# Performance work log

Measured on AMD Instinct MI355X. Metric: run time of the kernel, lower is better.

## Reference

```python
import jax, jax.numpy as jnp
import numpy as np

DT = 1.0 / 120.0
B, T = 2048, 2048


def setup_inputs() -> dict:
    key = jax.random.key(0)
    k1, k2 = jax.random.split(key)
    # friction, damping, restitution (restitution only affects the collision
    # branch, which is not exercised by the non-colliding reference dynamics)
    params = jax.random.uniform(k1, (3,), jnp.float32, 0.05, 0.9)
    # smooth synthetic trajectories: cumulative small steps of [x, y, theta]
    meas = jnp.cumsum(jax.random.normal(k2, (B, T, 3), jnp.float32) * 0.01, axis=1)
    return {"params": params, "measurements": meas}


def _ekf_loss(params, measurements):
    friction, damping = params[0], params[1]
    dt = jnp.asarray(DT, measurements.dtype)
    dtype = measurements.dtype

    R = jnp.diag(jnp.array([2.5e-7, 2.5e-7, 9.1e-3], dtype=dtype))
    Q = jnp.diag(jnp.array([2e-10, 2e-10, 3e-7, 3e-7, 1e-2, 1e-1], dtype=dtype))
    H = jnp.zeros((3, 6), dtype=dtype).at[0, 0].set(1.0).at[1, 1].set(1.0).at[2, 4].set(1.0)
    I6 = jnp.eye(6, dtype=dtype)

    # linearized transition Jacobian (constant-velocity with table damping)
    F = I6
    F = F.at[0, 2].set(dt).at[1, 3].set(dt).at[4, 5].set(dt)
    F = F.at[2, 2].set(1.0 - dt * damping).at[3, 3].set(1.0 - dt * damping)

    def predict_state(s):
        x, y, dx, dy, th, dth = s
        dx2 = dx - dt * (damping * dx + friction * jnp.sign(dx))
        dy2 = dy - dt * (damping * dy + friction * jnp.sign(dy))
        return jnp.stack([x + dx * dt, y + dy * dt, dx2, dy2, th + dth * dt, dth])

    def step(carry, z):
        s, P, acc = carry
        s_pred = predict_state(s)                     # (6,)
        P_pred = F @ P @ F.T + Q                      # (6,6)
        yv = z - H @ s_pred                           # (3,) innovation
        S = H @ P_pred @ H.T + R                      # (3,3)
        Sinv_y = jnp.linalg.solve(S, yv)
        K = jnp.linalg.solve(S.T, (P_pred @ H.T).T).T  # P_pred H^T S^{-1}
        s_new = s_pred + K @ yv
        P_new = (I6 - K @ H) @ P_pred
        # evaluation term: sign*exp(logdet(S)) + y^T S^{-1} y == det(S) + y^T S^{-1} y
        acc = acc + jnp.linalg.det(S) + yv @ Sinv_y
        return (s_new, P_new, acc), None

    def run_one(zs):
        # initial state from finite-difference velocities (as in the source)
        v0 = (zs[1] - zs[0]) / dt
        s0 = jnp.stack([zs[0, 0], zs[0, 1], v0[0], v0[1], zs[0, 2], v0[2]])
        P0 = I6 * 0.01
        (_, _, acc), _ = jax.lax.scan(step, (s0, P0, jnp.zeros((), dtype)), zs[1:])
        return acc / (zs.shape[0] - 1)

    return jnp.mean(jax.vmap(run_one)(measurements))


def reference(params, measurements):
    return _ekf_loss(params, measurements)
```

## Files before the change

kernel.cpp:

```cpp
#include <hip/hip_runtime.h>

#define DTF (1.0f/120.0f)

constexpr int Bn = 2048, Tn = 2048, NS = Tn - 1, ZF = Tn * 3;
constexpr int NCH = 16, LCH = 128;
constexpr int SPAN = 208;
constexpr int BT = 64;
constexpr int GX = Bn / BT;
constexpr int NBLK = GX * NCH;
constexpr int RING = 6;
constexpr int FR_F = 24;
constexpr int SLOT_F = BT * FR_F;

__global__ __launch_bounds__(BT, 2) void ekf_main(const float* __restrict__ params,
                                                  const float* __restrict__ meas,
                                                  double* __restrict__ part)
{
    __shared__ __align__(16) float lds[RING * SLOT_F];
    const int tid = threadIdx.x;
    const int B = blockIdx.x;
    const int m = (B & 7) * 64 + (B >> 3);
    const int g = m >> 4, c = m & 15;

    const float dt = DTF;
    const float fric = params[0];
    const float damping = params[1];
    const float a = 1.f - dt * damping;
    const float dfr = dt * fric;
    const float dt2 = dt * dt, a2 = a * a;
    const float qp = 2e-10f, qv = 3e-7f, qth = 1e-2f, qdth = 1e-1f;
    const float Rp = 2.5e-7f, Rt = 9.1e-3f;
    const char* __restrict__ ztb = (const char*)(meas + (size_t)(g * BT) * ZF);

    const int j0 = c * LCH;
    const int jend = min(j0 + LCH, NS);
    int jw = jend - SPAN;
    jw = (jw < 3) ? 0 : (jw - ((jw - 3) & 3));
    const int A0f = (3 * jw) & ~3;
    const int d = 3 * jw + 3 - A0f;
    const int r0 = j0 - jw, r1 = jend - jw;
    const bool head = (jw == 0);

    int Gbase[6], u16[6];
    #pragma unroll
    for (int i = 0; i < 6; ++i) {
        int U = i * 64 + tid;
        int rowL = U / 6, u = U - rowL * 6;
        int G = (rowL & 15) * 4 + (rowL >> 4);
        Gbase[i] = G * (ZF * 4);
        u16[i] = u * 16;
    }
    const int rbase = ((tid & 3) * 16 + (tid >> 2)) * FR_F;

#define ISSUE(F) do { \
    int As4_ = (A0f + 24 * (F)) * 4; \
    float* dst_ = &lds[((F) % RING) * SLOT_F]; \
    _Pragma("unroll") \
    for (int i_ = 0; i_ < 6; ++i_) { \
        int inrow_ = min(As4_ + u16[i_], (ZF - 4) * 4); \
        __builtin_amdgcn_global_load_lds((const void*)(ztb + Gbase[i_] + inrow_), \
                                         (void*)(dst_ + i_ * 256), 16, 0, 0); \
    } } while (0)

    ISSUE(0); ISSUE(1); ISSUE(2); ISSUE(3); ISSUE(4);

    float ckx0, ckx1, ckt0, ckt1, cisx, cist, cdet;
    {
        float x00=0.01f, x01=0.f, x11=0.01f, t00=0.01f, t01=0.f, t11=0.01f;
        for (int t = 0; t < 48; ++t) {
            float Pp00 = fmaf(dt2, x11, fmaf(2.f*dt, x01, x00)) + qp;
            float Pp01 = a * fmaf(dt, x11, x01);
            float Pp11 = fmaf(a2, x11, qv);
            float Sx = Pp00 + Rp, isx = __builtin_amdgcn_rcpf(Sx);
            float kx0 = Pp00*isx, kx1 = Pp01*isx;
            x00 = Pp00-kx0*Pp00; x01 = Pp01-kx0*Pp01; x11 = Pp11-kx1*Pp01;
            float Tp00 = fmaf(dt2, t11, fmaf(2.f*dt, t01, t00)) + qth;
            float Tp01 = fmaf(dt, t11, t01);
            float Tp11 = t11 + qdth;
            float St = Tp00 + Rt, ist = __builtin_amdgcn_rcpf(St);
            float kt0 = Tp00*ist, kt1 = Tp01*ist;
            t00 = Tp00-kt0*Tp00; t01 = Tp01-kt0*Tp01; t11 = Tp11-kt1*Tp01;
            ckx0=kx0; ckx1=kx1; ckt0=kt0; ckt1=kt1; cisx=isx; cist=ist; cdet=Sx*Sx*St;
        }
    }

    asm volatile("s_waitcnt vmcnt(24)" ::: "memory");
    __builtin_amdgcn_sched_barrier(0);

    const int ib = d - 3;
    float b0 = lds[rbase+ib], b1 = lds[rbase+ib+1], b2 = lds[rbase+ib+2];
    float b3 = lds[rbase+ib+3], b4 = lds[rbase+ib+4], b5 = lds[rbase+ib+5];
    float s0 = b0, s1 = b1, s4 = b2;
    float s2 = (b3-b0)/dt, s3 = (b4-b1)/dt, s5 = (b5-b2)/dt;

    float facc = 0.f, accP = 0.f, accT = 0.f;
    int nown = 0;
    float hx00=0.01f, hx01=0.f, hx11=0.01f, ht00=0.01f, ht01=0.f, ht11=0.01f;

    for (int s = 0;; ++s) {
        ISSUE(s + 5);
        asm volatile("s_waitcnt vmcnt(24)" ::: "memory");
        __builtin_amdgcn_sched_barrier(0);
        const float* sA = &lds[(s % RING) * SLOT_F + rbase];
        const float* sB = &lds[((s + 1) % RING) * SLOT_F + rbase];
        float zv[24];
        if (!head) {
            float4 v0 = *(const float4*)(sA + 4);
            float4 v1 = *(const float4*)(sA + 8);
            float4 v2 = *(const float4*)(sA + 12);
            float4 v3 = *(const float4*)(sA + 16);
            float4 v4 = *(const float4*)(sA + 20);
            float4 v5 = *(const float4*)(sB);
            zv[0]=v0.x; zv[1]=v0.y; zv[2]=v0.z; zv[3]=v0.w;
            zv[4]=v1.x; zv[5]=v1.y; zv[6]=v1.z; zv[7]=v1.w;
            zv[8]=v2.x; zv[9]=v2.y; zv[10]=v2.z; zv[11]=v2.w;
            zv[12]=v3.x; zv[13]=v3.y; zv[14]=v3.z; zv[15]=v3.w;
            zv[16]=v4.x; zv[17]=v4.y; zv[18]=v4.z; zv[19]=v4.w;
            zv[20]=v5.x; zv[21]=v5.y; zv[22]=v5.z; zv[23]=v5.w;
            #pragma unroll
            for (int ss = 0; ss < 8; ++ss) {
                float p0 = fmaf(dt, s2, s0), p1 = fmaf(dt, s3, s1), p4 = fmaf(dt, s5, s4);
                float p2 = fmaf(a, s2, -copysignf(dfr, s2));
                float p3 = fmaf(a, s3, -copysignf(dfr, s3));
                float y0 = zv[3*ss]-p0, y1 = zv[3*ss+1]-p1, y2 = zv[3*ss+2]-p4;
                s0 = fmaf(ckx0, y0, p0); s1 = fmaf(ckx0, y1, p1);
                s2 = fmaf(ckx1, y0, p2); s3 = fmaf(ckx1, y1, p3);
                s4 = fmaf(ckt0, y2, p4); s5 = fmaf(ckt1, y2, s5);
                int r = 8*s + ss;
                if (r >= r0 && r < r1) {
                    accP = fmaf(y0, y0, fmaf(y1, y1, accP));
                    accT = fmaf(y2, y2, accT);
                    ++nown;
                }
            }
        } else {
            #pragma unroll
            for (int k = 0; k < 21; ++k) zv[k] = sA[3 + k];
            zv[21] = sB[0]; zv[22] = sB[1]; zv[23] = sB[2];
            #pragma unroll
            for (int ss = 0; ss < 8; ++ss) {
                float Pp00 = fmaf(dt2, hx11, fmaf(2.f*dt, hx01, hx00)) + qp;
                float Pp01 = a * fmaf(dt, hx11, hx01);
                float Pp11 = fmaf(a2, hx11, qv);
                float Sx = Pp00 + Rp, isx = __builtin_amdgcn_rcpf(Sx);
                float kx0 = Pp00*isx, kx1 = Pp01*isx;
                hx00 = Pp00-kx0*Pp00; hx01 = Pp01-kx0*Pp01; hx11 = Pp11-kx1*Pp01;
                float Tp00 = fmaf(dt2, ht11, fmaf(2.f*dt, ht01, ht00)) + qth;
                float Tp01 = fmaf(dt, ht11, ht01);
                float Tp11 = ht11 + qdth;
                float St = Tp00 + Rt, ist = __builtin_amdgcn_rcpf(St);
                float kt0 = Tp00*ist, kt1 = Tp01*ist;
                ht00 = Tp00-kt0*Tp00; ht01 = Tp01-kt0*Tp01; ht11 = Tp11-kt1*Tp01;
                float p0 = fmaf(dt, s2, s0), p1 = fmaf(dt, s3, s1), p4 = fmaf(dt, s5, s4);
                float p2 = fmaf(a, s2, -copysignf(dfr, s2));
                float p3 = fmaf(a, s3, -copysignf(dfr, s3));
                float y0 = zv[3*ss]-p0, y1 = zv[3*ss+1]-p1, y2 = zv[3*ss+2]-p4;
                s0 = fmaf(kx0, y0, p0); s1 = fmaf(kx0, y1, p1);
                s2 = fmaf(kx1, y0, p2); s3 = fmaf(kx1, y1, p3);
                s4 = fmaf(kt0, y2, p4); s5 = fmaf(kt1, y2, s5);
                int r = 8*s + ss;
                if (r >= r0 && r < r1)
                    facc += Sx*Sx*St + isx*fmaf(y0, y0, y1*y1) + ist*y2*y2;
            }
        }
        if (8 * (s + 1) >= r1) break;
    }
    asm volatile("s_waitcnt vmcnt(0)" ::: "memory");
#undef ISSUE

    if (!head) facc = (float)nown * cdet + cisx * accP + cist * accT;

    double acc = (double)facc;
    for (int off = 32; off; off >>= 1) acc += __shfl_down(acc, off);
    if (tid == 0) part[m] = acc;
}

__global__ void finalize_kernel(const double* __restrict__ part, float* __restrict__ out)
{
    const int tid = threadIdx.x;
    double v = part[tid];
    for (int off = 32; off; off >>= 1) v += __shfl_down(v, off);
    __shared__ double wp[8];
    if ((tid & 63) == 0) wp[tid >> 6] = v;
    __syncthreads();
    if (tid == 0) {
        double t = 0.0;
        #pragma unroll
        for (int i = 0; i < 8; ++i) t += wp[i];
        out[0] = (float)(t / ((double)Bn * (double)NS));
    }
}

extern "C" void kernel_launch(void* const* d_in, const int* in_sizes, int n_in,
                              void* d_out, int out_size, void* d_ws, size_t ws_size,
                              hipStream_t stream)
{
    const float* params = (const float*)d_in[0];
    const float* meas = (const float*)d_in[1];
    double* part = (double*)d_ws;
    float* out = (float*)d_out;

    hipLaunchKernelGGL(ekf_main, dim3(NBLK), dim3(BT), 0, stream, params, meas, part);
    hipLaunchKernelGGL(finalize_kernel, dim3(1), dim3(512), 0, stream, part, out);
}
```

Before: 37.31 us.

## Share one staged measurement window between two waves per block with swizzled LDS

Blocks now have two wavefronts, and both consume the same 64-trajectory measurement window staged in LDS through a three-slot ring of 96-float frames. Each wave handles an overlapping 64-step sub-chunk with its own warm-up start, which shrinks the redundant warm-up span compared with the old 208-step window per 128-step chunk. The LDS layout uses an XOR swizzle so per-lane float4 reads avoid bank conflicts. The cost is block-level barriers around each frame, a cross-wave reduction, and uneven work between the exact head wave and the steady-state waves.

```diff
diff --git a/kernel.cpp b/kernel.cpp
--- a/kernel.cpp
+++ b/kernel.cpp
@@ -3,66 +3,56 @@
 #define DTF (1.0f/120.0f)
 
 constexpr int Bn = 2048, Tn = 2048, NS = Tn - 1, ZF = Tn * 3;
-constexpr int NCH = 16, LCH = 128;
-constexpr int SPAN = 208;
-constexpr int BT = 64;
-constexpr int GX = Bn / BT;
-constexpr int NBLK = GX * NCH;
-constexpr int RING = 6;
-constexpr int FR_F = 24;
-constexpr int SLOT_F = BT * FR_F;
+constexpr int NSUP = 16;
+constexpr int BT = 128;
+constexpr int NG = Bn / 64;
+constexpr int NBLK = NG * NSUP;
+constexpr int SLOT_F = 64 * 96;
 
 __global__ __launch_bounds__(BT, 2) void ekf_main(const float* __restrict__ params,
                                                   const float* __restrict__ meas,
                                                   double* __restrict__ part)
 {
-    __shared__ __align__(16) float lds[RING * SLOT_F];
-    const int tid = threadIdx.x;
+    __shared__ __align__(16) float lds[3 * SLOT_F];
+    __shared__ double wsum[2];
+
+    const int tid = threadIdx.x, wid = tid >> 6, lane = tid & 63;
     const int B = blockIdx.x;
-    const int m = (B & 7) * 64 + (B >> 3);
-    const int g = m >> 4, c = m & 15;
-
-    const float dt = DTF;
-    const float fric = params[0];
-    const float damping = params[1];
-    const float a = 1.f - dt * damping;
-    const float dfr = dt * fric;
+    const int g = (B & 7) + 8 * ((B >> 3) >> 4);
+    const int S = (B >> 3) & 15;
+    const int jz = 128 * S;
+    const int T_S = (S == 15) ? 4 : 6;
+
+    const float dt = DTF, fric = params[0], damping = params[1];
+    const float a = 1.f - dt * damping, dfr = dt * fric;
     const float dt2 = dt * dt, a2 = a * a;
     const float qp = 2e-10f, qv = 3e-7f, qth = 1e-2f, qdth = 1e-1f;
     const float Rp = 2.5e-7f, Rt = 9.1e-3f;
-    const char* __restrict__ ztb = (const char*)(meas + (size_t)(g * BT) * ZF);
-
-    const int j0 = c * LCH;
-    const int jend = min(j0 + LCH, NS);
-    int jw = jend - SPAN;
-    jw = (jw < 3) ? 0 : (jw - ((jw - 3) & 3));
-    const int A0f = (3 * jw) & ~3;
-    const int d = 3 * jw + 3 - A0f;
-    const int r0 = j0 - jw, r1 = jend - jw;
-    const bool head = (jw == 0);
-
-    int Gbase[6], u16[6];
+    const char* __restrict__ zb = (const char*)(meas + (size_t)g * 64 * ZF);
+
+    const bool exact = (S == 0 && wid == 0);
+    const int mst   = (S == 0 && wid == 1) ? 33 : (1 + 64 * wid);
+    const int mown0 = (S == 0) ? (wid ? 96 : 1) : (64 * (wid + 1));
+    const int mown1 = min((S == 0) ? (wid ? 192 : 96) : (64 * (wid + 2)), 2048 - jz);
+
+    int rbyte[12];
     #pragma unroll
-    for (int i = 0; i < 6; ++i) {
-        int U = i * 64 + tid;
-        int rowL = U / 6, u = U - rowL * 6;
-        int G = (rowL & 15) * 4 + (rowL >> 4);
-        Gbase[i] = G * (ZF * 4);
-        u16[i] = u * 16;
-    }
-    const int rbase = ((tid & 3) * 16 + (tid >> 2)) * FR_F;
+    for (int i = 0; i < 12; ++i) {
+        int ig = 12 * wid + i, C = 64 * ig + lane;
+        int r = C / 24, c = C - 24 * r;
+        rbyte[i] = r * (ZF * 4) + ((c ^ (r & 7)) * 16);
+    }
 
 #define ISSUE(F) do { \
-    int As4_ = (A0f + 24 * (F)) * 4; \
-    float* dst_ = &lds[((F) % RING) * SLOT_F]; \
+    int foff_ = (3 * jz + 96 * (F)) * 4; \
+    float* db_ = &lds[((F) % 3) * SLOT_F + wid * 12 * 256]; \
     _Pragma("unroll") \
-    for (int i_ = 0; i_ < 6; ++i_) { \
-        int inrow_ = min(As4_ + u16[i_], (ZF - 4) * 4); \
-        __builtin_amdgcn_global_load_lds((const void*)(ztb + Gbase[i_] + inrow_), \
-                                         (void*)(dst_ + i_ * 256), 16, 0, 0); \
-    } } while (0)
-
-    ISSUE(0); ISSUE(1); ISSUE(2); ISSUE(3); ISSUE(4);
+    for (int i_ = 0; i_ < 12; ++i_) \
+        __builtin_amdgcn_global_load_lds((const void*)(zb + rbyte[i_] + foff_), \
+                                         (void*)(db_ + i_ * 256), 16, 0, 0); \
+} while (0)
+
+    ISSUE(0); ISSUE(1); ISSUE(2);
 
     float ckx0, ckx1, ckt0, ckt1, cisx, cist, cdet;
     {
@@ -84,95 +74,100 @@
         }
     }
 
-    asm volatile("s_waitcnt vmcnt(24)" ::: "memory");
-    __builtin_amdgcn_sched_barrier(0);
-
-    const int ib = d - 3;
-    float b0 = lds[rbase+ib], b1 = lds[rbase+ib+1], b2 = lds[rbase+ib+2];
-    float b3 = lds[rbase+ib+3], b4 = lds[rbase+ib+4], b5 = lds[rbase+ib+5];
-    float s0 = b0, s1 = b1, s4 = b2;
-    float s2 = (b3-b0)/dt, s3 = (b4-b1)/dt, s5 = (b5-b2)/dt;
-
-    float facc = 0.f, accP = 0.f, accT = 0.f;
+    float s0=0.f,s1=0.f,s2=0.f,s3=0.f,s4=0.f,s5=0.f;
+    float hx00=0.01f,hx01=0.f,hx11=0.01f,ht00=0.01f,ht01=0.f,ht11=0.01f;
+    float facc=0.f, accP=0.f, accT=0.f;
     int nown = 0;
-    float hx00=0.01f, hx01=0.f, hx11=0.01f, ht00=0.01f, ht01=0.f, ht11=0.01f;
-
-    for (int s = 0;; ++s) {
-        ISSUE(s + 5);
-        asm volatile("s_waitcnt vmcnt(24)" ::: "memory");
-        __builtin_amdgcn_sched_barrier(0);
-        const float* sA = &lds[(s % RING) * SLOT_F + rbase];
-        const float* sB = &lds[((s + 1) % RING) * SLOT_F + rbase];
-        float zv[24];
-        if (!head) {
-            float4 v0 = *(const float4*)(sA + 4);
-            float4 v1 = *(const float4*)(sA + 8);
-            float4 v2 = *(const float4*)(sA + 12);
-            float4 v3 = *(const float4*)(sA + 16);
-            float4 v4 = *(const float4*)(sA + 20);
-            float4 v5 = *(const float4*)(sB);
-            zv[0]=v0.x; zv[1]=v0.y; zv[2]=v0.z; zv[3]=v0.w;
-            zv[4]=v1.x; zv[5]=v1.y; zv[6]=v1.z; zv[7]=v1.w;
-            zv[8]=v2.x; zv[9]=v2.y; zv[10]=v2.z; zv[11]=v2.w;
-            zv[12]=v3.x; zv[13]=v3.y; zv[14]=v3.z; zv[15]=v3.w;
-            zv[16]=v4.x; zv[17]=v4.y; zv[18]=v4.z; zv[19]=v4.w;
-            zv[20]=v5.x; zv[21]=v5.y; zv[22]=v5.z; zv[23]=v5.w;
-            #pragma unroll
-            for (int ss = 0; ss < 8; ++ss) {
-                float p0 = fmaf(dt, s2, s0), p1 = fmaf(dt, s3, s1), p4 = fmaf(dt, s5, s4);
-                float p2 = fmaf(a, s2, -copysignf(dfr, s2));
-                float p3 = fmaf(a, s3, -copysignf(dfr, s3));
-                float y0 = zv[3*ss]-p0, y1 = zv[3*ss+1]-p1, y2 = zv[3*ss+2]-p4;
-                s0 = fmaf(ckx0, y0, p0); s1 = fmaf(ckx0, y1, p1);
-                s2 = fmaf(ckx1, y0, p2); s3 = fmaf(ckx1, y1, p3);
-                s4 = fmaf(ckt0, y2, p4); s5 = fmaf(ckt1, y2, s5);
-                int r = 8*s + ss;
-                if (r >= r0 && r < r1) {
-                    accP = fmaf(y0, y0, fmaf(y1, y1, accP));
-                    accT = fmaf(y2, y2, accT);
-                    ++nown;
-                }
+    bool inited = false;
+    const int rx = lane & 7;
+
+#define PRED_UPD(KX0,KX1,KT0,KT1,Z0,Z1,Z2) \
+    float p0=fmaf(dt,s2,s0), p1=fmaf(dt,s3,s1), p4=fmaf(dt,s5,s4); \
+    float p2=fmaf(a,s2,-copysignf(dfr,s2)), p3=fmaf(a,s3,-copysignf(dfr,s3)); \
+    float y0=(Z0)-p0, y1=(Z1)-p1, y2=(Z2)-p4; \
+    s0=fmaf(KX0,y0,p0); s1=fmaf(KX0,y1,p1); s2=fmaf(KX1,y0,p2); s3=fmaf(KX1,y1,p3); \
+    s4=fmaf(KT0,y2,p4); s5=fmaf(KT1,y2,s5);
+
+#define TSTEP(K,Z0,Z1,Z2) { int m=m0+(K); if (m>=mst && m<mown1) { \
+    PRED_UPD(ckx0,ckx1,ckt0,ckt1,Z0,Z1,Z2) \
+    if (m>=mown0) { accP=fmaf(y0,y0,fmaf(y1,y1,accP)); accT=fmaf(y2,y2,accT); ++nown; } } }
+
+#define XSTEP(K,Z0,Z1,Z2) { int m=m0+(K); if (m>=mst && m<mown1) { \
+    float Pp00=fmaf(dt2,hx11,fmaf(2.f*dt,hx01,hx00))+qp; \
+    float Pp01=a*fmaf(dt,hx11,hx01); \
+    float Pp11=fmaf(a2,hx11,qv); \
+    float Sx=Pp00+Rp, isx=__builtin_amdgcn_rcpf(Sx); \
+    float kx0=Pp00*isx, kx1=Pp01*isx; \
+    hx00=Pp00-kx0*Pp00; hx01=Pp01-kx0*Pp01; hx11=Pp11-kx1*Pp01; \
+    float Tp00=fmaf(dt2,ht11,fmaf(2.f*dt,ht01,ht00))+qth; \
+    float Tp01=fmaf(dt,ht11,ht01); \
+    float Tp11=ht11+qdth; \
+    float St=Tp00+Rt, ist=__builtin_amdgcn_rcpf(St); \
+    float kt0=Tp00*ist, kt1=Tp01*ist; \
+    ht00=Tp00-kt0*Tp00; ht01=Tp01-kt0*Tp01; ht11=Tp11-kt1*Tp01; \
+    PRED_UPD(kx0,kx1,kt0,kt1,Z0,Z1,Z2) \
+    facc += Sx*Sx*St + isx*fmaf(y0,y0,y1*y1) + ist*y2*y2; } }
+
+#define READ6() \
+    float4 v0=*(const float4*)&fb[4*((cb+0)^rx)]; \
+    float4 v1=*(const float4*)&fb[4*((cb+1)^rx)]; \
+    float4 v2=*(const float4*)&fb[4*((cb+2)^rx)]; \
+    float4 v3=*(const float4*)&fb[4*((cb+3)^rx)]; \
+    float4 v4=*(const float4*)&fb[4*((cb+4)^rx)]; \
+    float4 v5=*(const float4*)&fb[4*((cb+5)^rx)]; \
+    if (!inited && m0 == mst-1) { \
+        s0=v0.x; s1=v0.y; s4=v0.z; \
+        s2=(v0.w-v0.x)/dt; s3=(v1.x-v0.y)/dt; s5=(v1.y-v0.z)/dt; inited=true; }
+
+    for (int f = 0; f < T_S; ++f) {
+        if (f <= T_S-3)      asm volatile("s_waitcnt vmcnt(24)" ::: "memory");
+        else if (f == T_S-2) asm volatile("s_waitcnt vmcnt(12)" ::: "memory");
+        else                 asm volatile("s_waitcnt vmcnt(0)"  ::: "memory");
+        __builtin_amdgcn_sched_barrier(0);
+        __builtin_amdgcn_s_barrier();
+        __builtin_amdgcn_sched_barrier(0);
+
+        const float* fb = &lds[(f % 3) * SLOT_F + lane * 96];
+        if (exact) {
+            for (int u = 0; u < 4; ++u) {
+                int m0 = 32*f + 8*u, cb = 6*u;
+                if (m0 + 8 <= mst-1 || m0 >= mown1) continue;
+                READ6()
+                XSTEP(0, v0.x,v0.y,v0.z)  XSTEP(1, v0.w,v1.x,v1.y)
+                XSTEP(2, v1.z,v1.w,v2.x)  XSTEP(3, v2.y,v2.z,v2.w)
+                XSTEP(4, v3.x,v3.y,v3.z)  XSTEP(5, v3.w,v4.x,v4.y)
+                XSTEP(6, v4.z,v4.w,v5.x)  XSTEP(7, v5.y,v5.z,v5.w)
             }
         } else {
-            #pragma unroll
-            for (int k = 0; k < 21; ++k) zv[k] = sA[3 + k];
-            zv[21] = sB[0]; zv[22] = sB[1]; zv[23] = sB[2];
-            #pragma unroll
-            for (int ss = 0; ss < 8; ++ss) {
-                float Pp00 = fmaf(dt2, hx11, fmaf(2.f*dt, hx01, hx00)) + qp;
-                float Pp01 = a * fmaf(dt, hx11, hx01);
-                float Pp11 = fmaf(a2, hx11, qv);
-                float Sx = Pp00 + Rp, isx = __builtin_amdgcn_rcpf(Sx);
-                float kx0 = Pp00*isx, kx1 = Pp01*isx;
-                hx00 = Pp00-kx0*Pp00; hx01 = Pp01-kx0*Pp01; hx11 = Pp11-kx1*Pp01;
-                float Tp00 = fmaf(dt2, ht11, fmaf(2.f*dt, ht01, ht00)) + qth;
-                float Tp01 = fmaf(dt, ht11, ht01);
-                float Tp11 = ht11 + qdth;
-                float St = Tp00 + Rt, ist = __builtin_amdgcn_rcpf(St);
-                float kt0 = Tp00*ist, kt1 = Tp01*ist;
-                ht00 = Tp00-kt0*Tp00; ht01 = Tp01-kt0*Tp01; ht11 = Tp11-kt1*Tp01;
-                float p0 = fmaf(dt, s2, s0), p1 = fmaf(dt, s3, s1), p4 = fmaf(dt, s5, s4);
-                float p2 = fmaf(a, s2, -copysignf(dfr, s2));
-                float p3 = fmaf(a, s3, -copysignf(dfr, s3));
-                float y0 = zv[3*ss]-p0, y1 = zv[3*ss+1]-p1, y2 = zv[3*ss+2]-p4;
-                s0 = fmaf(kx0, y0, p0); s1 = fmaf(kx0, y1, p1);
-                s2 = fmaf(kx1, y0, p2); s3 = fmaf(kx1, y1, p3);
-                s4 = fmaf(kt0, y2, p4); s5 = fmaf(kt1, y2, s5);
-                int r = 8*s + ss;
-                if (r >= r0 && r < r1)
-                    facc += Sx*Sx*St + isx*fmaf(y0, y0, y1*y1) + ist*y2*y2;
+            for (int u = 0; u < 4; ++u) {
+                int m0 = 32*f + 8*u, cb = 6*u;
+                if (m0 + 8 <= mst-1 || m0 >= mown1) continue;
+                READ6()
+                TSTEP(0, v0.x,v0.y,v0.z)  TSTEP(1, v0.w,v1.x,v1.y)
+                TSTEP(2, v1.z,v1.w,v2.x)  TSTEP(3, v2.y,v2.z,v2.w)
+                TSTEP(4, v3.x,v3.y,v3.z)  TSTEP(5, v3.w,v4.x,v4.y)
+                TSTEP(6, v4.z,v4.w,v5.x)  TSTEP(7, v5.y,v5.z,v5.w)
             }
         }
-        if (8 * (s + 1) >= r1) break;
+        __builtin_amdgcn_sched_barrier(0);
+        __builtin_amdgcn_s_barrier();
+        __builtin_amdgcn_sched_barrier(0);
+        if (f + 3 < T_S) ISSUE(f + 3);
     }
     asm volatile("s_waitcnt vmcnt(0)" ::: "memory");
+
+#undef READ6
+#undef XSTEP
+#undef TSTEP
+#undef PRED_UPD
 #undef ISSUE
 
-    if (!head) facc = (float)nown * cdet + cisx * accP + cist * accT;
-
-    double acc = (double)facc;
+    float ft = exact ? facc : (float)nown * cdet + cisx * accP + cist * accT;
+    double acc = (double)ft;
     for (int off = 32; off; off >>= 1) acc += __shfl_down(acc, off);
-    if (tid == 0) part[m] = acc;
+    if (lane == 0) wsum[wid] = acc;
+    __syncthreads();
+    if (tid == 0) part[B] = wsum[0] + wsum[1];
 }
 
 __global__ void finalize_kernel(const double* __restrict__ part, float* __restrict__ out)
```

Measured after the change: 37.70 us. No clear change (+1.0%).
